# Performance work log

Measured on AMD Instinct MI355X. Metric: run time of the kernel, lower is better.

The kernel has to match this reference:

```python
import jax, jax.numpy as jnp
import numpy as np

N_FRAMES = 4
HEADS = 8
SEQ = 576
DIM = 640


def setup_inputs() -> dict:
    key = jax.random.key(0)
    ks = jax.random.split(key, 6)
    x = jax.random.normal(ks[0], (3 * N_FRAMES, SEQ, DIM), dtype=jnp.float32)
    s = 1.0 / np.sqrt(DIM)
    Wq = jax.random.normal(ks[1], (DIM, DIM), dtype=jnp.float32) * s
    Wk = jax.random.normal(ks[2], (DIM, DIM), dtype=jnp.float32) * s
    Wv = jax.random.normal(ks[3], (DIM, DIM), dtype=jnp.float32) * s
    Wo = jax.random.normal(ks[4], (DIM, DIM), dtype=jnp.float32) * s
    bo = jnp.zeros((DIM,), dtype=jnp.float32)
    return {"x": x, "Wq": Wq, "Wk": Wk, "Wv": Wv, "Wo": Wo, "bo": bo}


def reference(x, Wq, Wk, Wv, Wo, bo):
    # x: [3F, S, D] -- stacked [source | uncond | cond] frame batches
    B, S, D = x.shape
    n = B // 3                       # n_frames
    h = HEADS
    hd = D // h
    scale = 1.0 / jnp.sqrt(jnp.asarray(hd, x.dtype))

    # torch nn.Linear: y = x @ W.T
    q = jnp.einsum('bsd,ed->bse', x, Wq)
    k = jnp.einsum('bsd,ed->bse', x, Wk)
    v = jnp.einsum('bsd,ed->bse', x, Wv)

    def heads_fd(t):  # [F,S,D] -> [F,h,S,hd]
        return t.reshape(t.shape[0], S, h, hd).transpose(0, 2, 1, 3)

    def heads_flat(t):  # [F,S,D] -> [h, F*S, hd]  (shared across all query frames)
        return t.reshape(t.shape[0] * S, h, hd).transpose(1, 0, 2)

    # ---- source: per-frame self-attention ----
    qs, ks_, vs = heads_fd(q[:n]), heads_fd(k[:n]), heads_fd(v[:n])
    sim_s = jnp.einsum('fhqd,fhkd->fhqk', qs, ks_) * scale
    out_s = jnp.einsum('fhqk,fhkd->fhqd', jax.nn.softmax(sim_s, axis=-1), vs)

    # ---- uncond / cond: each frame attends to concatenated KV of all frames ----
    def cross_frame(q_chunk, k_chunk, v_chunk):
        qf = heads_fd(q_chunk)          # [F,h,S,hd]
        kf = heads_flat(k_chunk)        # [h,F*S,hd]
        vf = heads_flat(v_chunk)        # [h,F*S,hd]
        sim = jnp.einsum('fhqd,hkd->fhqk', qf, kf) * scale   # [F,h,S,F*S]
        return jnp.einsum('fhqk,hkd->fhqd', jax.nn.softmax(sim, axis=-1), vf)

    out_u = cross_frame(q[n:2 * n], k[n:2 * n], v[n:2 * n])
    out_c = cross_frame(q[2 * n:], k[2 * n:], v[2 * n:])

    out = jnp.concatenate([out_s, out_u, out_c], axis=0)      # [3F,h,S,hd]
    out = out.transpose(0, 2, 1, 3).reshape(B, S, D)          # merge heads
    return jnp.einsum('bsd,ed->bse', out, Wo) + bo
```

## Files before the change

### kernel.cpp

```cpp
#include <hip/hip_runtime.h>
#include <hip/hip_bf16.h>

#define SEQ    576
#define DIM    640
#define HEADS  8
#define HD     80
#define NF     4
#define NB     12
#define M_TOT  (NB * SEQ)
#define SCALE  0.11180339887498949f
#define LOG2E  1.4426950408889634f

typedef __attribute__((ext_vector_type(8))) short          bf16x8;
typedef __attribute__((ext_vector_type(4))) float          f32x4;
typedef __attribute__((ext_vector_type(8))) unsigned short u16x8;
typedef __attribute__((ext_vector_type(4))) unsigned short u16x4;

__device__ __forceinline__ unsigned short f2bf(float x) {
    unsigned u = __float_as_uint(x);
    u += 0x7fffu + ((u >> 16) & 1u);
    return (unsigned short)(u >> 16);
}
__device__ __forceinline__ float bf2f(unsigned short h) {
    return __uint_as_float((unsigned)h << 16);
}
__device__ __forceinline__ f32x4 mfma16(bf16x8 a, bf16x8 b, f32x4 c) {
    return __builtin_amdgcn_mfma_f32_16x16x32_bf16(a, b, c, 0, 0, 0);
}
__device__ __forceinline__ float fexp2(float x) {
    return __builtin_amdgcn_exp2f(x);
}
__device__ __forceinline__ void dma16(const void* g, void* s) {
    __builtin_amdgcn_global_load_lds(
        (const __attribute__((address_space(1))) void*)g,
        (__attribute__((address_space(3))) void*)s, 16, 0, 0);
}

__global__ __launch_bounds__(256) void split_kernel(
    const float* __restrict__ X,  const float* __restrict__ Wq,
    const float* __restrict__ Wk, const float* __restrict__ Wv,
    const float* __restrict__ Wo,
    unsigned short* __restrict__ Xh,  unsigned short* __restrict__ Wqh,
    unsigned short* __restrict__ Wkh, unsigned short* __restrict__ Wvh,
    unsigned short* __restrict__ Woh)
{
    const int z = blockIdx.y;
    const float* src; unsigned short* dh; int n; float s = 1.0f;
    switch (z) {
        case 0:  src = X;  dh = Xh;  n = M_TOT * DIM; break;
        case 1:  src = Wq; dh = Wqh; n = DIM * DIM; s = SCALE * LOG2E; break;
        case 2:  src = Wk; dh = Wkh; n = DIM * DIM; break;
        case 3:  src = Wv; dh = Wvh; n = DIM * DIM; break;
        default: src = Wo; dh = Woh; n = DIM * DIM; break;
    }
    const int base = blockIdx.x * 4096 + threadIdx.x * 16;
    if (base >= n) return;
#pragma unroll
    for (int half = 0; half < 2; ++half) {
        const int b = base + half * 8;
        float4 a4 = *(const float4*)(src + b);
        float4 b4 = *(const float4*)(src + b + 4);
        float vv[8] = {a4.x, a4.y, a4.z, a4.w, b4.x, b4.y, b4.z, b4.w};
        union { unsigned short u[8]; u16x8 v; } ph;
#pragma unroll
        for (int j = 0; j < 8; ++j) ph.u[j] = f2bf(vv[j] * s);
        *(u16x8*)(dh + b) = ph.v;
    }
}

__global__ __launch_bounds__(256) void qkv_mfma_kernel(
    const unsigned short* __restrict__ Xh,
    const unsigned short* __restrict__ Wqh, const unsigned short* __restrict__ Wkh,
    const unsigned short* __restrict__ Wvh,
    unsigned short* __restrict__ Qh,
    unsigned short* __restrict__ Kb, unsigned short* __restrict__ VtG)
{
    __shared__ unsigned short smem[2][10240];

    const int flat = blockIdx.x + 27 * (blockIdx.y + 10 * blockIdx.z);
    const int xcd  = flat & 7;
    const int slot = flat >> 3;
    const int l    = (xcd < 2 ? xcd * 102 : 204 + (xcd - 2) * 101) + slot;
    const int m_idx = l / 30;
    const int rem   = l - m_idx * 30;
    const int z     = rem / 10;
    const int n_idx = rem - z * 10;

    const unsigned short* WH = (z == 0) ? Wqh : ((z == 1) ? Wkh : Wvh);
    const int m0 = m_idx * 256;
    const int n0 = n_idx * 64;

    const int t    = threadIdx.x;
    const int w    = t >> 6;
    const int lane = t & 63;
    const int quad = lane >> 4;
    const int ln   = lane & 15;

    f32x4 acc[4][4];
#pragma unroll
    for (int mi = 0; mi < 4; ++mi)
#pragma unroll
        for (int nt = 0; nt < 4; ++nt)
#pragma unroll
            for (int e = 0; e < 4; ++e) acc[mi][nt][e] = 0.f;

    const int lr = lane >> 2;
    const int lc = (lane & 3) * 8;

    auto stage = [&](int buf, int k0) {
        unsigned short* As = smem[buf];
        unsigned short* Bs = smem[buf] + 8192;
        const unsigned short* gp = Xh + (size_t)(m0 + w * 64 + lr) * DIM + k0 + lc;
#pragma unroll
        for (int i = 0; i < 4; ++i)
            dma16(gp + (size_t)i * 16 * DIM, &As[(w * 64 + i * 16) * 32]);
        const size_t gb = (size_t)(n0 + w * 16 + lr) * DIM + k0 + lc;
        dma16(WH + gb, &Bs[w * 16 * 32]);
    };

    stage(0, 0);
    __syncthreads();

    for (int k0 = 0; k0 < DIM; k0 += 32) {
        const int kb = (k0 >> 5) & 1;
        if (k0 + 32 < DIM) stage(kb ^ 1, k0 + 32);

        const unsigned short* As = smem[kb];
        const unsigned short* Bs = smem[kb] + 8192;
        bf16x8 af[4];
#pragma unroll
        for (int mi = 0; mi < 4; ++mi)
            af[mi] = *(const bf16x8*)&As[(w * 64 + mi * 16 + ln) * 32 + quad * 8];
#pragma unroll
        for (int nt = 0; nt < 4; ++nt) {
            bf16x8 bh = *(const bf16x8*)&Bs[(nt * 16 + ln) * 32 + quad * 8];
#pragma unroll
            for (int mi = 0; mi < 4; ++mi)
                acc[mi][nt] = mfma16(af[mi], bh, acc[mi][nt]);
        }
        __syncthreads();
    }

    if (z == 0) {
#pragma unroll
        for (int mi = 0; mi < 4; ++mi)
#pragma unroll
            for (int r = 0; r < 4; ++r) {
                const size_t row = m0 + w * 64 + mi * 16 + quad * 4 + r;
#pragma unroll
                for (int nt = 0; nt < 4; ++nt)
                    Qh[row * DIM + n0 + nt * 16 + ln] = f2bf(acc[mi][nt][r]);
            }
    } else if (z == 1) {
#pragma unroll
        for (int mi = 0; mi < 4; ++mi)
#pragma unroll
            for (int r = 0; r < 4; ++r) {
                const size_t row = m0 + w * 64 + mi * 16 + quad * 4 + r;
#pragma unroll
                for (int nt = 0; nt < 4; ++nt)
                    Kb[row * DIM + n0 + nt * 16 + ln] = f2bf(acc[mi][nt][r]);
            }
    } else {
        unsigned short* Vts = smem[0];
#pragma unroll 1
        for (int half = 0; half < 2; ++half) {
            __syncthreads();
            if ((w >> 1) == half) {
                const int wl = w & 1;
#pragma unroll
                for (int mi = 0; mi < 4; ++mi)
#pragma unroll
                    for (int nt = 0; nt < 4; ++nt)
#pragma unroll
                        for (int r = 0; r < 4; ++r)
                            Vts[(nt * 16 + ln) * 136 + wl * 64 + mi * 16 + quad * 4 + r] =
                                f2bf(acc[mi][nt][r]);
            }
            __syncthreads();
            const int nn = t & 63;
            const int c0 = (t >> 6) * 32;
#pragma unroll
            for (int i = 0; i < 4; ++i)
                *(u16x8*)(VtG + (size_t)(n0 + nn) * M_TOT + m0 + half * 128 + c0 + i * 8) =
                    *(const u16x8*)&Vts[nn * 136 + c0 + i * 8];
        }
    }
}

__global__ __launch_bounds__(256, 2) void attn_mfma_kernel(
    const unsigned short* __restrict__ Qh,
    const unsigned short* __restrict__ Kb, const unsigned short* __restrict__ Vt,
    unsigned short* __restrict__ Oh,
    unsigned short* __restrict__ Pn, float2* __restrict__ ml)
{
    const int flat = blockIdx.x + 3 * (blockIdx.y + 8 * blockIdx.z);
    const int h    = flat & 7;
    const int slot = flat >> 3;
    const int z    = slot / 3;
    const int qt   = slot - z * 3;

    int f, kbase, nkt, idx = -1;
    if (z < 16) {
        idx = z;
        const int fi = z >> 1;
        f = 4 + fi;
        kbase = ((fi < 4 ? 4 : 8) + (z & 1) * 2) * SEQ;
        nkt = 18;
    } else {
        f = z - 16;
        kbase = f * SEQ;
        nkt = 9;
    }

    const int t    = threadIdx.x;
    const int w    = t >> 6;
    const int lane = t & 63;
    const int quad = lane >> 4;
    const int ln   = lane & 15;

    __shared__ unsigned short KhS[2][64 * 96];
    __shared__ unsigned short VtS[2][80 * 64];
    __shared__ unsigned short Pb[4 * 48 * 72];

    bf16x8 qf[3][3];
#pragma unroll
    for (int mi = 0; mi < 3; ++mi) {
        const int qrow = f * SEQ + qt * 192 + w * 48 + mi * 16 + ln;
        const unsigned short* qp = Qh + (size_t)qrow * DIM + h * HD;
#pragma unroll
        for (int kc = 0; kc < 3; ++kc) {
            const int dbase = kc * 32 + quad * 8;
            if (dbase < HD) {
                qf[mi][kc] = *(const bf16x8*)(qp + dbase);
            } else {
                union { unsigned short u[8]; bf16x8 v; } zz;
#pragma unroll
                for (int j = 0; j < 8; ++j) zz.u[j] = 0;
                qf[mi][kc] = zz.v;
            }
        }
    }

    auto stage_k = [&](int buf, int kvt) {
        const unsigned short* kg = Kb + (size_t)(kbase + kvt * 64) * DIM + h * HD;
#pragma unroll
        for (int rnd = 0; rnd < 3; ++rnd) {
            const int unit = rnd * 256 + t;
            const int kr = unit / 12, kc = unit % 12;
            dma16(kg + (size_t)kr * DIM + kc * 8,
                  &KhS[buf][(rnd * 256 + w * 64) * 8]);
        }
    };
    u16x8 vreg[3];
    auto load_v = [&](int kvt) {
#pragma unroll
        for (int i = 0; i < 3; ++i) {
            const int u = t + i * 256;
            if (u < 640) {
                const int d = u >> 3, c8 = u & 7;
                vreg[i] = *(const u16x8*)(Vt + (size_t)(h * HD + d) * M_TOT +
                                          kbase + kvt * 64 + c8 * 8);
            }
        }
    };
    auto write_v = [&](int buf) {
#pragma unroll
        for (int i = 0; i < 3; ++i) {
            const int u = t + i * 256;
            if (u < 640) {
                const int d = u >> 3, c8 = u & 7;
                const int c8s = (c8 + 3 * d) & 7;
                *(u16x8*)&VtS[buf][d * 64 + c8s * 8] = vreg[i];
            }
        }
    };

    float m_[3], l_[3];
#pragma unroll
    for (int mi = 0; mi < 3; ++mi) { m_[mi] = -INFINITY; l_[mi] = 0.f; }

    f32x4 oacc[3][5];
#pragma unroll
    for (int mi = 0; mi < 3; ++mi)
#pragma unroll
        for (int nt = 0; nt < 5; ++nt)
#pragma unroll
            for (int e = 0; e < 4; ++e) oacc[mi][nt][e] = 0.f;

    unsigned short* PbW = &Pb[w * 48 * 72];

    stage_k(0, 0);
    load_v(0);
    write_v(0);
    __syncthreads();

    for (int kt = 0; kt < nkt; ++kt) {
        const int cur = kt & 1;
        const bool pf = (kt + 1 < nkt);

        if (pf) {
            load_v(kt + 1);
            stage_k(cur ^ 1, kt + 1);
        }

        f32x4 sacc[3][4];
#pragma unroll
        for (int mi = 0; mi < 3; ++mi)
#pragma unroll
            for (int nt = 0; nt < 4; ++nt)
#pragma unroll
                for (int e = 0; e < 4; ++e) sacc[mi][nt][e] = 0.f;
#pragma unroll
        for (int nt = 0; nt < 4; ++nt)
#pragma unroll
            for (int kc = 0; kc < 3; ++kc) {
                bf16x8 kf = *(const bf16x8*)&KhS[cur][(nt * 16 + ln) * 96 + kc * 32 + quad * 8];
#pragma unroll
                for (int mi = 0; mi < 3; ++mi)
                    sacc[mi][nt] = mfma16(kf, qf[mi][kc], sacc[mi][nt]);
            }

        float aq[3];
#pragma unroll
        for (int mi = 0; mi < 3; ++mi) {
            float mx = sacc[mi][0][0];
#pragma unroll
            for (int nt = 0; nt < 4; ++nt)
#pragma unroll
                for (int r = 0; r < 4; ++r) mx = fmaxf(mx, sacc[mi][nt][r]);
            mx = fmaxf(mx, __shfl_xor(mx, 16));
            mx = fmaxf(mx, __shfl_xor(mx, 32));
            const float mnew = fmaxf(m_[mi], mx);
            aq[mi] = fexp2(m_[mi] - mnew);
            m_[mi] = mnew;
            float s = 0.f;
#pragma unroll
            for (int nt = 0; nt < 4; ++nt) {
                union { unsigned short u[4]; u16x4 v; } pk;
#pragma unroll
                for (int r = 0; r < 4; ++r) {
                    const float p = fexp2(sacc[mi][nt][r] - m_[mi]);
                    s += p;
                    pk.u[r] = (unsigned short)(__float_as_uint(p) >> 16);
                }
                *(u16x4*)&PbW[(mi * 16 + ln) * 72 + nt * 16 + quad * 4] = pk.v;
            }
            s += __shfl_xor(s, 16);
            s += __shfl_xor(s, 32);
            l_[mi] = l_[mi] * aq[mi] + s;
        }

#pragma unroll
        for (int mi = 0; mi < 3; ++mi)
#pragma unroll
            for (int r = 0; r < 4; ++r) {
                const float ar = __shfl(aq[mi], quad * 4 + r, 64);
#pragma unroll
                for (int nt = 0; nt < 5; ++nt) oacc[mi][nt][r] *= ar;
            }

        __threadfence_block();

#pragma unroll
        for (int kc = 0; kc < 2; ++kc) {
            bf16x8 pf_[3];
#pragma unroll
            for (int mi = 0; mi < 3; ++mi)
                pf_[mi] = *(const bf16x8*)&PbW[(mi * 16 + ln) * 72 + kc * 32 + quad * 8];
#pragma unroll
            for (int nt = 0; nt < 5; ++nt) {
                const int vrow = nt * 16 + ln;
                const int c8r  = ((kc * 4 + quad) + 3 * vrow) & 7;
                bf16x8 vf = *(const bf16x8*)&VtS[cur][vrow * 64 + c8r * 8];
#pragma unroll
                for (int mi = 0; mi < 3; ++mi)
                    oacc[mi][nt] = mfma16(pf_[mi], vf, oacc[mi][nt]);
            }
        }

        if (pf) write_v(cur ^ 1);
        __syncthreads();
    }

#pragma unroll
    for (int mi = 0; mi < 3; ++mi)
#pragma unroll
        for (int r = 0; r < 4; ++r) {
            const float lr_ = __shfl(l_[mi], quad * 4 + r, 64);
            const float inv = 1.f / lr_;
            const int rr = qt * 192 + w * 48 + mi * 16 + quad * 4 + r;
            if (idx < 0) {
                const size_t orow = (size_t)f * SEQ + rr;
#pragma unroll
                for (int nt = 0; nt < 5; ++nt)
                    Oh[orow * DIM + h * HD + nt * 16 + ln] = f2bf(oacc[mi][nt][r] * inv);
            } else {
#pragma unroll
                for (int nt = 0; nt < 5; ++nt)
                    Pn[((size_t)idx * SEQ + rr) * DIM + h * HD + nt * 16 + ln] =
                        f2bf(oacc[mi][nt][r] * inv);
            }
        }
    if (idx >= 0 && lane < 16) {
#pragma unroll
        for (int mi = 0; mi < 3; ++mi) {
            const int rr = qt * 192 + w * 48 + mi * 16 + lane;
            ml[((size_t)idx * 8 + h) * SEQ + rr] = make_float2(m_[mi], l_[mi]);
        }
    }
}

__global__ __launch_bounds__(320) void merge_kernel(
    const unsigned short* __restrict__ Pn, const float2* __restrict__ ml,
    unsigned short* __restrict__ Oh)
{
    const int row = blockIdx.x;
    const int fi  = blockIdx.y;
    const int t   = threadIdx.x;
    const int i0  = fi * 2, i1 = i0 + 1;
#pragma unroll
    for (int rep = 0; rep < 2; ++rep) {
        const int col = t + rep * 320;
        const int h = col / 80;
        const float2 a = ml[((size_t)i0 * 8 + h) * SEQ + row];
        const float2 b = ml[((size_t)i1 * 8 + h) * SEQ + row];
        const float M  = fmaxf(a.x, b.x);
        const float w0 = fexp2(a.x - M) * a.y;
        const float w1 = fexp2(b.x - M) * b.y;
        const float inv = 1.f / (w0 + w1);
        const float p0 = bf2f(Pn[((size_t)i0 * SEQ + row) * DIM + col]);
        const float p1 = bf2f(Pn[((size_t)i1 * SEQ + row) * DIM + col]);
        Oh[((size_t)(4 + fi) * SEQ + row) * DIM + col] = f2bf((w0 * p0 + w1 * p1) * inv);
    }
}

__global__ __launch_bounds__(256) void oproj_mfma_kernel(
    const unsigned short* __restrict__ Oh,
    const unsigned short* __restrict__ Woh,
    const float* __restrict__ bo, float* __restrict__ out)
{
    __shared__ unsigned short smem[2][10240];

    const int flat = blockIdx.x + 27 * blockIdx.y;
    const int xcd  = flat & 7;
    const int slot = flat >> 3;
    const int l    = (xcd < 6 ? xcd * 34 : 204 + (xcd - 6) * 33) + slot;
    const int m_idx = l / 10;
    const int n_idx = l - m_idx * 10;
    const int m0 = m_idx * 256;
    const int n0 = n_idx * 64;

    const int t    = threadIdx.x;
    const int w    = t >> 6;
    const int lane = t & 63;
    const int quad = lane >> 4;
    const int ln   = lane & 15;

    f32x4 acc[4][4];
#pragma unroll
    for (int mi = 0; mi < 4; ++mi)
#pragma unroll
        for (int nt = 0; nt < 4; ++nt)
#pragma unroll
            for (int e = 0; e < 4; ++e) acc[mi][nt][e] = 0.f;

    const int lr = lane >> 2;
    const int lc = (lane & 3) * 8;

    auto stage = [&](int buf, int k0) {
        unsigned short* As = smem[buf];
        unsigned short* Bs = smem[buf] + 8192;
        const unsigned short* gp = Oh + (size_t)(m0 + w * 64 + lr) * DIM + k0 + lc;
#pragma unroll
        for (int i = 0; i < 4; ++i)
            dma16(gp + (size_t)i * 16 * DIM, &As[(w * 64 + i * 16) * 32]);
        const size_t gb = (size_t)(n0 + w * 16 + lr) * DIM + k0 + lc;
        dma16(Woh + gb, &Bs[w * 16 * 32]);
    };

    stage(0, 0);
    __syncthreads();

    for (int k0 = 0; k0 < DIM; k0 += 32) {
        const int kb = (k0 >> 5) & 1;
        if (k0 + 32 < DIM) stage(kb ^ 1, k0 + 32);

        const unsigned short* As = smem[kb];
        const unsigned short* Bs = smem[kb] + 8192;
        bf16x8 af[4];
#pragma unroll
        for (int mi = 0; mi < 4; ++mi)
            af[mi] = *(const bf16x8*)&As[(w * 64 + mi * 16 + ln) * 32 + quad * 8];
#pragma unroll
        for (int nt = 0; nt < 4; ++nt) {
            bf16x8 bh = *(const bf16x8*)&Bs[(nt * 16 + ln) * 32 + quad * 8];
#pragma unroll
            for (int mi = 0; mi < 4; ++mi)
                acc[mi][nt] = mfma16(af[mi], bh, acc[mi][nt]);
        }
        __syncthreads();
    }

#pragma unroll
    for (int mi = 0; mi < 4; ++mi)
#pragma unroll
        for (int r = 0; r < 4; ++r) {
            const size_t row = m0 + w * 64 + mi * 16 + quad * 4 + r;
#pragma unroll
            for (int nt = 0; nt < 4; ++nt) {
                const int col = n0 + nt * 16 + ln;
                out[row * DIM + col] = acc[mi][nt][r] + bo[col];
            }
        }
}

extern "C" void kernel_launch(void* const* d_in, const int* in_sizes, int n_in,
                              void* d_out, int out_size, void* d_ws, size_t ws_size,
                              hipStream_t stream)
{
    const float* x  = (const float*)d_in[0];
    const float* Wq = (const float*)d_in[1];
    const float* Wk = (const float*)d_in[2];
    const float* Wv = (const float*)d_in[3];
    const float* Wo = (const float*)d_in[4];
    const float* bo = (const float*)d_in[5];
    float* out = (float*)d_out;

    const size_t NX = (size_t)M_TOT * DIM;
    const size_t NW = (size_t)DIM * DIM;
    unsigned short* p = (unsigned short*)d_ws;
    unsigned short* Wqh = p;  p += NW;
    unsigned short* Wkh = p;  p += NW;
    unsigned short* Wvh = p;  p += NW;
    unsigned short* Woh = p;  p += NW;
    unsigned short* Xh  = p;  p += NX;
    unsigned short* Qhb = p;  p += NX;
    unsigned short* Kbb = p;  p += NX;
    unsigned short* Vtb = p;  p += NX;
    unsigned short* Ohb = Xh;

    unsigned short* Pn = (unsigned short*)d_out;
    float2* ml = (float2*)((char*)d_out + (size_t)16 * SEQ * DIM * 2);

    dim3 g0((unsigned)((NX + 4095) / 4096), 5);
    split_kernel<<<g0, 256, 0, stream>>>(x, Wq, Wk, Wv, Wo,
        Xh, Wqh, Wkh, Wvh, Woh);

    dim3 g1(M_TOT / 256, DIM / 64, 3);
    qkv_mfma_kernel<<<g1, 256, 0, stream>>>(Xh, Wqh, Wkh, Wvh, Qhb, Kbb, Vtb);

    dim3 g2(3, HEADS, 20);
    attn_mfma_kernel<<<g2, 256, 0, stream>>>(Qhb, Kbb, Vtb, Ohb, Pn, ml);

    dim3 g3(SEQ, 8);
    merge_kernel<<<g3, 320, 0, stream>>>(Pn, ml, Ohb);

    dim3 g4(M_TOT / 256, DIM / 64);
    oproj_mfma_kernel<<<g4, 256, 0, stream>>>(Ohb, Woh, bo, out);
}
```

Baseline: 193.3 us.

## Skip lazy softmax rescaling, defer row-sum reduction, and restripe K smem layout

Only rescales the running max and output accumulators when some lane's tile max exceeds the stored max by more than a threshold, checked with a wave-wide any. The cross-lane row-sum reduction moves out of the loop to the epilogue, and float-to-bf16 packing now uses a byte-permute instruction. The K tile shared-memory layout changes to a column-group-major arrangement so each DMA writes contiguous 512-element chunks, aiming to reduce bank conflicts and address arithmetic. Deferred rescaling risks larger exponent values but stays bounded by the threshold.

After: 191.1 us. About the same (-1.1%).

```diff
diff --git a/kernel.cpp b/kernel.cpp
--- a/kernel.cpp
+++ b/kernel.cpp
@@ -219,7 +219,7 @@
     const int quad = lane >> 4;
     const int ln   = lane & 15;
 
-    __shared__ unsigned short KhS[2][64 * 96];
+    __shared__ unsigned short KhS[2][12 * 64 * 8];
     __shared__ unsigned short VtS[2][80 * 64];
     __shared__ unsigned short Pb[4 * 48 * 72];
 
@@ -246,10 +246,8 @@
         const unsigned short* kg = Kb + (size_t)(kbase + kvt * 64) * DIM + h * HD;
 #pragma unroll
         for (int rnd = 0; rnd < 3; ++rnd) {
-            const int unit = rnd * 256 + t;
-            const int kr = unit / 12, kc = unit % 12;
-            dma16(kg + (size_t)kr * DIM + kc * 8,
-                  &KhS[buf][(rnd * 256 + w * 64) * 8]);
+            const int g = rnd * 4 + w;
+            dma16(kg + (size_t)lane * DIM + g * 8, &KhS[buf][g * 512]);
         }
     };
     u16x8 vreg[3];
@@ -315,50 +313,61 @@
         for (int nt = 0; nt < 4; ++nt)
 #pragma unroll
             for (int kc = 0; kc < 3; ++kc) {
-                bf16x8 kf = *(const bf16x8*)&KhS[cur][(nt * 16 + ln) * 96 + kc * 32 + quad * 8];
+                bf16x8 kf = *(const bf16x8*)&KhS[cur][((kc * 4 + quad) * 64 +
+                                                      nt * 16 + ln) * 8];
 #pragma unroll
                 for (int mi = 0; mi < 3; ++mi)
                     sacc[mi][nt] = mfma16(kf, qf[mi][kc], sacc[mi][nt]);
             }
 
-        float aq[3];
+        float mxl[3];
 #pragma unroll
         for (int mi = 0; mi < 3; ++mi) {
-            float mx = sacc[mi][0][0];
+            float t0[4];
 #pragma unroll
             for (int nt = 0; nt < 4; ++nt)
-#pragma unroll
-                for (int r = 0; r < 4; ++r) mx = fmaxf(mx, sacc[mi][nt][r]);
-            mx = fmaxf(mx, __shfl_xor(mx, 16));
-            mx = fmaxf(mx, __shfl_xor(mx, 32));
-            const float mnew = fmaxf(m_[mi], mx);
-            aq[mi] = fexp2(m_[mi] - mnew);
-            m_[mi] = mnew;
+                t0[nt] = fmaxf(fmaxf(sacc[mi][nt][0], sacc[mi][nt][1]),
+                               fmaxf(sacc[mi][nt][2], sacc[mi][nt][3]));
+            mxl[mi] = fmaxf(fmaxf(t0[0], t0[1]), fmaxf(t0[2], t0[3]));
+        }
+        const bool need = (mxl[0] > m_[0] + 8.0f) || (mxl[1] > m_[1] + 8.0f) ||
+                          (mxl[2] > m_[2] + 8.0f);
+        if (__any(need)) {
+#pragma unroll
+            for (int mi = 0; mi < 3; ++mi) {
+                float mx = fmaxf(mxl[mi], __shfl_xor(mxl[mi], 16));
+                mx = fmaxf(mx, __shfl_xor(mx, 32));
+                const float mnew = fmaxf(m_[mi], mx);
+                const float aq = fexp2(m_[mi] - mnew);
+                m_[mi] = mnew;
+                l_[mi] *= aq;
+#pragma unroll
+                for (int r = 0; r < 4; ++r) {
+                    const float ar = __shfl(aq, quad * 4 + r, 64);
+#pragma unroll
+                    for (int nt = 0; nt < 5; ++nt) oacc[mi][nt][r] *= ar;
+                }
+            }
+        }
+#pragma unroll
+        for (int mi = 0; mi < 3; ++mi) {
             float s = 0.f;
 #pragma unroll
             for (int nt = 0; nt < 4; ++nt) {
-                union { unsigned short u[4]; u16x4 v; } pk;
-#pragma unroll
-                for (int r = 0; r < 4; ++r) {
-                    const float p = fexp2(sacc[mi][nt][r] - m_[mi]);
-                    s += p;
-                    pk.u[r] = (unsigned short)(__float_as_uint(p) >> 16);
-                }
+                const float p0 = fexp2(sacc[mi][nt][0] - m_[mi]);
+                const float p1 = fexp2(sacc[mi][nt][1] - m_[mi]);
+                const float p2 = fexp2(sacc[mi][nt][2] - m_[mi]);
+                const float p3 = fexp2(sacc[mi][nt][3] - m_[mi]);
+                s += (p0 + p1) + (p2 + p3);
+                union { unsigned u32[2]; u16x4 v; } pk;
+                pk.u32[0] = __builtin_amdgcn_perm(__float_as_uint(p1),
+                                                  __float_as_uint(p0), 0x07060302u);
+                pk.u32[1] = __builtin_amdgcn_perm(__float_as_uint(p3),
+                                                  __float_as_uint(p2), 0x07060302u);
                 *(u16x4*)&PbW[(mi * 16 + ln) * 72 + nt * 16 + quad * 4] = pk.v;
             }
-            s += __shfl_xor(s, 16);
-            s += __shfl_xor(s, 32);
-            l_[mi] = l_[mi] * aq[mi] + s;
-        }
-
-#pragma unroll
-        for (int mi = 0; mi < 3; ++mi)
-#pragma unroll
-            for (int r = 0; r < 4; ++r) {
-                const float ar = __shfl(aq[mi], quad * 4 + r, 64);
-#pragma unroll
-                for (int nt = 0; nt < 5; ++nt) oacc[mi][nt][r] *= ar;
-            }
+            l_[mi] += s;
+        }
 
         __threadfence_block();
 
@@ -383,6 +392,11 @@
         __syncthreads();
     }
 
+#pragma unroll
+    for (int mi = 0; mi < 3; ++mi) {
+        l_[mi] += __shfl_xor(l_[mi], 16);
+        l_[mi] += __shfl_xor(l_[mi], 32);
+    }
 #pragma unroll
     for (int mi = 0; mi < 3; ++mi)
 #pragma unroll
```
